# Kernel tuning notes

Hardware: AMD Instinct MI355X
Metric: run time of the kernel (lower is better)

## Reference

```python
import jax, jax.numpy as jnp
import numpy as np
from jax import lax

B, L, D, VOCAB = 4, 256, 256, 29


def conv1d(x, w, b, pad, stride=1):
    # x: (B, C, Len), w: (O, I, K)
    y = lax.conv_general_dilated(x, w, (stride,), [pad], dimension_numbers=('NCH', 'OIH', 'NCH'))
    return y + b[None, :, None]


def setup_inputs() -> dict:
    key = jax.random.key(0)
    ks = jax.random.split(key, 14)
    n = lambda k, shape: jax.random.normal(k, shape, jnp.float32) * 0.05
    return {
        'prot_data1': jax.random.randint(ks[0], (B, L), 0, VOCAB),
        'prot_data2': jax.random.randint(ks[1], (B, L), 0, VOCAB),
        'emb': n(ks[2], (VOCAB, D)),
        'w0': n(ks[3], (D, D, 4)), 'b0': jnp.zeros((D,), jnp.float32),
        'w1': n(ks[4], (D, D, 8)), 'b1': jnp.zeros((D,), jnp.float32),
        'w2': n(ks[5], (D, D, 12)), 'b2': jnp.zeros((D,), jnp.float32),
        'ja1_w': n(ks[6], (D, D)), 'ja1_b': jnp.zeros((D,), jnp.float32),
        'ja2_w': n(ks[7], (D, D)), 'ja2_b': jnp.zeros((D,), jnp.float32),
        'rc_w': n(ks[8], (64, 1, 4)), 'rc_b': jnp.zeros((64,), jnp.float32),
        'fc1_w': n(ks[9], (64 * 32, 600)), 'fc1_b': jnp.zeros((600,), jnp.float32),
        'fc2_w': n(ks[10], (600, 300)), 'fc2_b': jnp.zeros((300,), jnp.float32),
        'fc3_w': n(ks[11], (300, 1)), 'fc3_b': jnp.zeros((1,), jnp.float32),
    }


def reference(prot_data1, prot_data2, emb, w0, b0, w1, b1, w2, b2,
              ja1_w, ja1_b, ja2_w, ja2_b, rc_w, rc_b,
              fc1_w, fc1_b, fc2_w, fc2_b, fc3_w, fc3_b):
    lrelu = lambda x: jnp.where(x >= 0, x, 0.1 * x)

    def encode(tok):
        x = emb[tok]  # (B, L, D); dim 1 is treated as conv channels, as in original
        x = jax.nn.relu(conv1d(x, w0, b0, (1, 2)))
        x = jax.nn.relu(conv1d(x, w1, b1, (3, 4)))
        x = jax.nn.relu(conv1d(x, w2, b2, (5, 6)))
        return x  # (B, L, D), length preserved

    e1 = encode(prot_data1)
    e2 = encode(prot_data2)

    q = jax.nn.relu(e1) @ ja1_w + ja1_b  # (B, L, D)
    k = jax.nn.relu(e2) @ ja2_w + ja2_b  # (B, L, D)
    inter = jax.nn.sigmoid(jnp.einsum('bij,bkj->bik', q, k))  # (B, L, L)
    inter = inter / jnp.sum(inter, axis=(1, 2), keepdims=True)

    # bilinear cross-attention pooling: tanh outer product weighted by inter
    pp = jnp.tanh(e1[:, :, None, :] * e2[:, None, :, :])  # (B, L, L, D)
    pooled = jnp.einsum('bikj,bik->bj', pp, inter)  # (B, D)

    h = lrelu(conv1d(pooled[:, None, :], rc_w, rc_b, (1, 1), stride=2))  # (B, 64, 128)
    h = h.reshape(h.shape[0], 64, 32, 4).max(axis=-1)  # MaxPool1d(4,4) -> (B, 64, 32)
    h = h.reshape(h.shape[0], 64 * 32)
    h = lrelu(h @ fc1_w + fc1_b)
    h = lrelu(h @ fc2_w + fc2_b)
    affn = h @ fc3_w + fc3_b  # (B, 1)
    return (inter, affn)
```

## Files before the change

kernel.cpp:

```cpp
#include <hip/hip_runtime.h>
#include <hip/hip_bf16.h>

typedef unsigned short u16;
typedef unsigned int u32;
typedef short s8v __attribute__((ext_vector_type(8)));
typedef float f32x16 __attribute__((ext_vector_type(16)));

constexpr int B = 4, L = 256, D = 256;
constexpr size_t SZ = (size_t)B * L * D;

constexpr int XROWS = 272;
constexpr size_t XT_PLANE = (size_t)8 * XROWS * 256;

constexpr size_t OFF_E    = 0;
constexpr size_t OFF_S    = 2 * SZ;
constexpr size_t OFF_EBF  = 3 * SZ;
constexpr size_t OFF_XA   = 4 * SZ;
constexpr size_t OFF_XB   = OFF_XA + 278528;
constexpr size_t OFF_WB   = OFF_XB + 278528;
constexpr size_t OFF_WJ   = OFF_WB + 1572864;
constexpr size_t OFF_QK   = OFF_WJ + 131072;
constexpr size_t OFF_BS   = OFF_QK + 262144;
constexpr size_t OFF_PP   = OFF_BS + 256;
constexpr size_t OFF_POOL = OFF_PP + 524288;
constexpr size_t OFF_H    = OFF_POOL + 1024;
constexpr size_t OFF_F1P  = OFF_H + 8192;
constexpr size_t OFF_F2P  = OFF_F1P + 76800;

constexpr size_t WB_L1 = 0;
constexpr size_t WB_L2 = (size_t)4 * 2 * 65536;
constexpr size_t WB_L3 = WB_L2 + (size_t)8 * 2 * 65536;

__device__ __forceinline__ float sig_fast(float x) {
  return __fdividef(1.0f, 1.0f + __expf(-x));
}
__device__ __forceinline__ float lrelu(float x) { return x >= 0.0f ? x : 0.1f * x; }

__device__ __forceinline__ void split_bf16(float v, u16& h, u16& l) {
  __bf16 hb = (__bf16)v;
  float hf = (float)hb;
  __bf16 lb = (__bf16)(v - hf);
  h = __builtin_bit_cast(u16, hb);
  l = __builtin_bit_cast(u16, lb);
}
__device__ __forceinline__ u16 to_bf16(float v) {
  return __builtin_bit_cast(u16, (__bf16)v);
}

__device__ __forceinline__ s8v lds16_8al(const u16* p) {
  union { uint2 u[2]; s8v v; } r;
  r.u[0] = *(const uint2*)p;
  r.u[1] = *(const uint2*)(p + 4);
  return r.v;
}

__global__ __launch_bounds__(256) void k_prepall(const int* __restrict__ t1,
                                                 const int* __restrict__ t2,
                                                 const float* __restrict__ emb,
                                                 const float* __restrict__ w0,
                                                 const float* __restrict__ w1,
                                                 const float* __restrict__ w2,
                                                 const float* __restrict__ jw1,
                                                 const float* __restrict__ jw2,
                                                 u16* __restrict__ xa,
                                                 u16* __restrict__ xb,
                                                 u16* __restrict__ wb,
                                                 u16* __restrict__ wj) {
  __shared__ float st[32][129];
  int blk = blockIdx.x;
  int t = threadIdx.x;
  if (blk < 64) {
    int gid = blk * 256 + t;
    int plane = gid >> 13, rem = gid & 8191;
    int pb = rem >> 10, rem2 = rem & 1023;
    int row16 = rem2 >> 6, cc = rem2 & 63;
    int row = row16 < 8 ? row16 : 256 + row16;
    u16* dst = plane ? xb : xa;
    *(ushort4*)(dst + (size_t)pb * (XROWS * 256) + (size_t)row * 256 + cc * 4) =
        make_ushort4(0, 0, 0, 0);
  } else if (blk < 896) {
    int b2 = blk - 64;
    if (b2 < 768) {
      const float* w; u16* dst; int K, lblk;
      if (b2 < 128) { w = w0; dst = wb + WB_L1; K = 4; lblk = b2; }
      else if (b2 < 384) { w = w1; dst = wb + WB_L2; K = 8; lblk = b2 - 128; }
      else { w = w2; dst = wb + WB_L3; K = 12; lblk = b2 - 384; }
      int q = lblk >> 5, ig = lblk & 31, oc = t;
      union { u16 us[8]; uint4 v; } H, Lo;
#pragma unroll
      for (int e = 0; e < 8; ++e) {
        float v = w[((size_t)oc * 256 + ig * 8 + e) * K + q];
        split_bf16(v, H.us[e], Lo.us[e]);
      }
      size_t d = (size_t)(q * 2) * 65536 + (size_t)ig * 2048 + (size_t)oc * 8;
      *(uint4*)(dst + d) = H.v;
      *(uint4*)(dst + d + 65536) = Lo.v;
    } else {
      int lblk = b2 - 768;
      int kg = lblk & 31, p = lblk >> 5;
      const float* W = p ? jw2 : jw1;
      int n = t;
      union { u16 us[8]; uint4 v; } H, Lo;
#pragma unroll
      for (int e = 0; e < 8; ++e) {
        float v = W[(size_t)(kg * 8 + e) * 256 + n];
        split_bf16(v, H.us[e], Lo.us[e]);
      }
      size_t d = (size_t)(p * 2) * 65536 + ((size_t)kg * 256 + n) * 8;
      *(uint4*)(wj + d) = H.v;
      *(uint4*)(wj + d + 65536) = Lo.v;
    }
  } else {
    int lb = blk - 896;
    int dt = lb & 1, lt = (lb >> 1) & 7, pb = lb >> 4;
    int l0 = lt * 32, d0 = dt * 128;
    const int* tok = (pb >> 2) ? t2 : t1;
    int c = t & 127, rq = t >> 7;
#pragma unroll 4
    for (int rr = 0; rr < 16; ++rr) {
      int r = rr * 2 + rq;
      int tv = tok[(pb & 3) * 256 + l0 + r];
      st[r][c] = emb[(size_t)tv * 256 + d0 + c];
    }
    __syncthreads();
    int dloc = t >> 1, lq = t & 1;
    size_t rbase = (size_t)pb * (XROWS * 256) + (size_t)(8 + d0 + dloc) * 256 + l0 + lq * 16;
#pragma unroll
    for (int lh = 0; lh < 4; ++lh) {
      u16 hb[4];
#pragma unroll
      for (int cc = 0; cc < 4; ++cc)
        hb[cc] = to_bf16(st[lq * 16 + lh * 4 + cc][dloc]);
      *(ushort4*)(xa + rbase + lh * 4) = make_ushort4(hb[0], hb[1], hb[2], hb[3]);
    }
  }
}

template <int K, int P, int OUTMODE>
__global__ __launch_bounds__(256, 2) void k_cmf(const u16* __restrict__ xh,
                                                const u16* __restrict__ wb,
                                                const float* __restrict__ bias,
                                                u16* __restrict__ yh,
                                                float* __restrict__ eout,
                                                u16* __restrict__ ebf) {
  __shared__ u16 xsl[4 * 3264];
  __shared__ float cd[3072];

  int blk = blockIdx.x;
  int jt = blk & 7, oct = (blk >> 3) & 7, pb = blk >> 6;
  int oc0 = oct * 32, j0 = jt * 32;
  int tid = threadIdx.x;
  int lane = tid & 63, wv = tid >> 6;
  int l31 = lane & 31, lhi = lane >> 5;

  {
    const u16* src = xh + (size_t)pb * (XROWS * 256) + (size_t)j0 * 256 + wv * 64;
    u16* dst = xsl + wv * 3264;
#pragma unroll
    for (int it2 = 0; it2 < 12; ++it2) {
      int e = it2 * 64 + lane;
      int r = e >> 4, c4 = (e & 15) * 4;
      *(uint2*)(dst + r * 68 + c4) = *(const uint2*)(src + (size_t)r * 256 + c4);
    }
  }
  asm volatile("s_waitcnt lgkmcnt(0)" ::: "memory");
  __builtin_amdgcn_sched_barrier(0);

  f32x16 acc = {};
  size_t abase = (size_t)(oc0 + l31) * 8 + (size_t)(wv * 8 + lhi) * 2048;
  const u16* wslice = xsl + wv * 3264 + 8 * lhi;

  for (int q = 0; q < K; ++q) {
    int jr = l31 + q + (8 - P);
    const u16* bh0 = wslice + jr * 68;
    size_t aq = (size_t)q * 131072 + abase;
#pragma unroll
    for (int ic = 0; ic < 4; ++ic) {
      s8v ah = *(const s8v*)(wb + aq + ic * 4096);
      s8v al = *(const s8v*)(wb + aq + 65536 + ic * 4096);
      s8v bh = lds16_8al(bh0 + ic * 16);
      acc = __builtin_amdgcn_mfma_f32_32x32x16_bf16(ah, bh, acc, 0, 0, 0);
      acc = __builtin_amdgcn_mfma_f32_32x32x16_bf16(al, bh, acc, 0, 0, 0);
    }
  }

  if (wv > 0) {
#pragma unroll
    for (int r = 0; r < 16; ++r) {
      int ocr = (r & 3) + 8 * (r >> 2) + 4 * lhi;
      cd[(wv - 1) * 1024 + ocr * 32 + l31] = acc[r];
    }
  }
  __syncthreads();
  if (wv == 0) {
    float v[16];
#pragma unroll
    for (int r = 0; r < 16; ++r) {
      int ocr = (r & 3) + 8 * (r >> 2) + 4 * lhi;
      int idx = ocr * 32 + l31;
      v[r] = fmaxf(acc[r] + cd[idx] + cd[1024 + idx] + cd[2048 + idx] + bias[oc0 + ocr], 0.0f);
    }
    if constexpr (OUTMODE == 0) {
      size_t ro = (size_t)pb * (XROWS * 256) + (size_t)(8 + j0 + l31) * 256 + oc0 + 4 * lhi;
#pragma unroll
      for (int rq = 0; rq < 4; ++rq) {
        *(ushort4*)(yh + ro + 8 * rq) =
            make_ushort4(to_bf16(v[rq * 4 + 0]), to_bf16(v[rq * 4 + 1]),
                         to_bf16(v[rq * 4 + 2]), to_bf16(v[rq * 4 + 3]));
      }
    } else {
#pragma unroll
      for (int r = 0; r < 16; ++r) {
        int ocr = (r & 3) + 8 * (r >> 2) + 4 * lhi;
        size_t eo = (size_t)pb * 65536 + (size_t)(oc0 + ocr) * 256 + j0 + l31;
        eout[eo] = v[r];
        ebf[((size_t)pb * 256 + oc0 + ocr) * 256 + j0 + l31] = to_bf16(v[r]);
      }
    }
  }
}

__global__ __launch_bounds__(256) void k_jam(const u16* __restrict__ ebf,
                                             const u16* __restrict__ wj,
                                             const float* __restrict__ b1,
                                             const float* __restrict__ b2,
                                             u16* __restrict__ qk) {
  __shared__ float cd[3072 + 1056];
  int blk = blockIdx.x;
  int nt = blk & 7, it = (blk >> 3) & 7, pb = blk >> 6;
  int p = pb >> 2;
  int i0 = it * 32, n0 = nt * 32;
  int tid = threadIdx.x, wv = tid >> 6, lane = tid & 63;
  int l31 = lane & 31, lhi = lane >> 5;

  const u16* eh = ebf + ((size_t)pb * 256 + i0 + l31) * 256 + lhi * 8;
  const u16* wjh = wj + (size_t)(p * 2) * 65536;

  f32x16 acc = {};
#pragma unroll
  for (int c = 0; c < 4; ++c) {
    int kc = wv * 4 + c;
    int kg = kc * 2 + lhi;
    s8v ah = *(const s8v*)(eh + kc * 16);
    s8v bh = *(const s8v*)(wjh + ((size_t)kg * 256 + n0 + l31) * 8);
    s8v bl = *(const s8v*)(wjh + 65536 + ((size_t)kg * 256 + n0 + l31) * 8);
    acc = __builtin_amdgcn_mfma_f32_32x32x16_bf16(ah, bh, acc, 0, 0, 0);
    acc = __builtin_amdgcn_mfma_f32_32x32x16_bf16(ah, bl, acc, 0, 0, 0);
  }

  if (wv > 0) {
#pragma unroll
    for (int r = 0; r < 16; ++r) {
      int row = (r & 3) + 8 * (r >> 2) + 4 * lhi;
      cd[(wv - 1) * 1024 + row * 32 + l31] = acc[r];
    }
  }
  __syncthreads();
  if (wv == 0) {
    float bv = (p ? b2 : b1)[n0 + l31];
#pragma unroll
    for (int r = 0; r < 16; ++r) {
      int row = (r & 3) + 8 * (r >> 2) + 4 * lhi;
      int idx = row * 32 + l31;
      cd[3072 + row * 33 + l31] = acc[r] + cd[idx] + cd[1024 + idx] + cd[2048 + idx] + bv;
    }
  }
  __syncthreads();

  int row = tid & 31, c8 = tid >> 5;
  u16 hb[4];
#pragma unroll
  for (int cc = 0; cc < 4; ++cc)
    hb[cc] = to_bf16(cd[3072 + row * 33 + c8 * 4 + cc]);
  size_t ro = ((size_t)pb * 256 + i0 + row) * 256 + n0 + c8 * 4;
  *(ushort4*)(qk + ro) = make_ushort4(hb[0], hb[1], hb[2], hb[3]);
}

__global__ __launch_bounds__(256) void k_scoresm(const u16* __restrict__ qk,
                                                 float* __restrict__ S,
                                                 float* __restrict__ bsums) {
  __shared__ float cd[3072 + 1056];
  int blk = blockIdx.x;
  int jt = blk & 7, it = (blk >> 3) & 7, b = blk >> 6;
  int i0 = it * 32, j0 = jt * 32;
  int tid = threadIdx.x, wv = tid >> 6, lane = tid & 63;
  int l31 = lane & 31, lhi = lane >> 5;

  const u16* qh = qk + ((size_t)b * 256 + i0 + l31) * 256 + lhi * 8;
  const u16* kh = qk + ((size_t)(4 + b) * 256 + j0 + l31) * 256 + lhi * 8;

  f32x16 acc = {};
#pragma unroll
  for (int c = 0; c < 4; ++c) {
    int kc = wv * 4 + c;
    s8v a = *(const s8v*)(qh + kc * 16);
    s8v bb = *(const s8v*)(kh + kc * 16);
    acc = __builtin_amdgcn_mfma_f32_32x32x16_bf16(a, bb, acc, 0, 0, 0);
  }

  if (wv > 0) {
#pragma unroll
    for (int r = 0; r < 16; ++r) {
      int row = (r & 3) + 8 * (r >> 2) + 4 * lhi;
      cd[(wv - 1) * 1024 + row * 32 + l31] = acc[r];
    }
  }
  __syncthreads();
  if (wv == 0) {
    float psum = 0.0f;
#pragma unroll
    for (int r = 0; r < 16; ++r) {
      int row = (r & 3) + 8 * (r >> 2) + 4 * lhi;
      int idx = row * 32 + l31;
      float s = sig_fast(acc[r] + cd[idx] + cd[1024 + idx] + cd[2048 + idx]);
      psum += s;
      cd[3072 + row * 33 + l31] = s;
    }
    for (int off = 32; off; off >>= 1) psum += __shfl_down(psum, off, 64);
    if (lane == 0) bsums[blk] = psum;
  }
  __syncthreads();

  int row = tid & 31, c8 = tid >> 5;
  float4 v;
  v.x = cd[3072 + row * 33 + c8 * 4 + 0];
  v.y = cd[3072 + row * 33 + c8 * 4 + 1];
  v.z = cd[3072 + row * 33 + c8 * 4 + 2];
  v.w = cd[3072 + row * 33 + c8 * 4 + 3];
  *(float4*)(S + ((size_t)b * 256 + i0 + row) * 256 + j0 + c8 * 4) = v;
}

__global__ __launch_bounds__(256) void k_pool(const float* __restrict__ e1,
                                              const float* __restrict__ e2,
                                              const float* __restrict__ S,
                                              const float* __restrict__ bsums,
                                              float* __restrict__ inter_out,
                                              float* __restrict__ pp) {
  int blk = blockIdx.x;
  int kch = blk & 15, ich = (blk >> 4) & 31, b = blk >> 9;
  int d = threadIdx.x, i0 = ich * 8, k0 = kch * 16;
  __shared__ float s2[16][8];
  __shared__ float red[128];
  __shared__ float ssp_s, tot_s;
  int t = threadIdx.x;
  int ii = t >> 4, kk = t & 15;
  float sv = 0.0f;
  if (t < 64) {
    float v = bsums[b * 64 + t];
    for (int off = 32; off; off >>= 1) v += __shfl_down(v, off, 64);
    if (t == 0) tot_s = v;
  }
  if (t < 128) {
    sv = S[((size_t)(b * 256 + i0 + ii)) * 256 + k0 + kk];
    s2[kk][ii] = 2.0f * sv;
    red[t] = sv;
  }
  __syncthreads();
  for (int st = 64; st; st >>= 1) {
    if (t < st) red[t] += red[t + st];
    __syncthreads();
  }
  if (t == 0) ssp_s = red[0];
  __syncthreads();

  float invt = 1.0f / tot_s;
  if (t < 128)
    inter_out[((size_t)(b * 256 + i0 + ii)) * 256 + k0 + kk] = sv * invt;

  constexpr float C2L = 2.8853900817779268f;
  float ev2[8];
#pragma unroll
  for (int i2 = 0; i2 < 8; ++i2)
    ev2[i2] = e1[((size_t)(b * L + i0 + i2)) * D + d] * C2L;

  float a0 = 0.f, a1 = 0.f, a2 = 0.f, a3 = 0.f;
  for (int k2 = 0; k2 < 16; ++k2) {
    float e2v = e2[((size_t)(b * L + k0 + k2)) * D + d];
    float s2r[8];
    *(float4*)&s2r[0] = *(const float4*)&s2[k2][0];
    *(float4*)&s2r[4] = *(const float4*)&s2[k2][4];
#pragma unroll
    for (int i2 = 0; i2 < 8; ++i2) {
      float r = __builtin_amdgcn_rcpf(__builtin_exp2f(ev2[i2] * e2v) + 1.0f);
      if ((i2 & 3) == 0) a0 = fmaf(r, s2r[i2], a0);
      else if ((i2 & 3) == 1) a1 = fmaf(r, s2r[i2], a1);
      else if ((i2 & 3) == 2) a2 = fmaf(r, s2r[i2], a2);
      else a3 = fmaf(r, s2r[i2], a3);
    }
  }
  float res = (ssp_s - (a0 + a1 + a2 + a3)) * invt;
  pp[(((size_t)b * 32 + ich) * 16 + kch) * 256 + d] = res;
}

__global__ __launch_bounds__(256) void k_poolcomb(const float* __restrict__ pp,
                                                  float* __restrict__ pooled) {
  int blk = blockIdx.x;
  int dt = blk & 7, b = blk >> 3;
  int t = threadIdx.x, dl = t & 31, mg = t >> 5;
  int d = dt * 32 + dl;
  float s = 0.f;
#pragma unroll
  for (int m = 0; m < 64; ++m)
    s += pp[((size_t)b * 512 + mg * 64 + m) * 256 + d];
  __shared__ float red[8][32];
  red[mg][dl] = s;
  __syncthreads();
  if (mg == 0) {
    float tot = red[0][dl] + red[1][dl] + red[2][dl] + red[3][dl] +
                red[4][dl] + red[5][dl] + red[6][dl] + red[7][dl];
    pooled[b * 256 + d] = tot;
  }
}

__global__ __launch_bounds__(256) void k_head1(const float* __restrict__ pooled,
                                               const float* __restrict__ rcw,
                                               const float* __restrict__ rcb,
                                               float* __restrict__ h) {
  int ms = blockIdx.x;
  __shared__ float spb[4][258];
  int t = threadIdx.x;
#pragma unroll
  for (int s = 0; s < 4; ++s) {
    int idx = s * 256 + t;
    spb[idx >> 8][(idx & 255) + 1] = pooled[idx];
  }
  if (t < 4) { spb[t][0] = 0.0f; spb[t][257] = 0.0f; }
  __syncthreads();
  int b = t >> 6, c = t & 63;
  float w0 = rcw[c * 4 + 0], w1 = rcw[c * 4 + 1], w2 = rcw[c * 4 + 2], w3 = rcw[c * 4 + 3];
  float bias = rcb[c];
#pragma unroll
  for (int mm = 0; mm < 4; ++mm) {
    int m = ms * 4 + mm;
    float mx = -1e30f;
#pragma unroll
    for (int r = 0; r < 4; ++r) {
      int p2 = 2 * (4 * m + r);
      float y = bias;
      y = fmaf(w0, spb[b][p2], y);
      y = fmaf(w1, spb[b][p2 + 1], y);
      y = fmaf(w2, spb[b][p2 + 2], y);
      y = fmaf(w3, spb[b][p2 + 3], y);
      mx = fmaxf(mx, lrelu(y));
    }
    h[(size_t)(b * 64 + c) * 32 + m] = mx;
  }
}

__global__ __launch_bounds__(256) void k_fc1(const float* __restrict__ h,
                                             const float* __restrict__ w,
                                             float* __restrict__ f1p) {
  int blk = blockIdx.x;
  int ich = blk & 31, ot = blk >> 5;
  int t = threadIdx.x, ol = t & 63, b = t >> 6;
  int o = ot * 64 + ol;
  int oc_ = o < 600 ? o : 599;
  const float* hb = h + (size_t)b * 2048 + ich * 64;
  const float* wb = w + (size_t)(ich * 64) * 600 + oc_;
  float a0 = 0.f, a1 = 0.f, a2 = 0.f, a3 = 0.f;
#pragma unroll 4
  for (int i = 0; i < 64; i += 4) {
    a0 = fmaf(hb[i], wb[(size_t)i * 600], a0);
    a1 = fmaf(hb[i + 1], wb[(size_t)(i + 1) * 600], a1);
    a2 = fmaf(hb[i + 2], wb[(size_t)(i + 2) * 600], a2);
    a3 = fmaf(hb[i + 3], wb[(size_t)(i + 3) * 600], a3);
  }
  if (o < 600) f1p[((size_t)ich * 4 + b) * 600 + o] = a0 + a1 + a2 + a3;
}

__global__ __launch_bounds__(256) void k_fc2(const float* __restrict__ f1p,
                                             const float* __restrict__ fc1b,
                                             const float* __restrict__ w,
                                             float* __restrict__ f2p) {
  int blk = blockIdx.x;
  int is = blk & 7, ot = blk >> 3;
  __shared__ float h1s[4][76];
  int t = threadIdx.x;
  for (int e = t; e < 300; e += 256) {
    int bb = e / 75, ii = e % 75;
    int i = is * 75 + ii;
    float s = fc1b[i];
#pragma unroll
    for (int ich = 0; ich < 32; ++ich) s += f1p[((size_t)ich * 4 + bb) * 600 + i];
    h1s[bb][ii] = lrelu(s);
  }
  __syncthreads();
  int ol = t & 63, b = t >> 6;
  int o = ot * 64 + ol, oc_ = o < 300 ? o : 299;
  const float* wb = w + (size_t)(is * 75) * 300 + oc_;
  float a0 = 0.f, a1 = 0.f, a2 = 0.f;
#pragma unroll 5
  for (int ii = 0; ii < 75; ii += 3) {
    a0 = fmaf(h1s[b][ii], wb[(size_t)ii * 300], a0);
    a1 = fmaf(h1s[b][ii + 1], wb[(size_t)(ii + 1) * 300], a1);
    a2 = fmaf(h1s[b][ii + 2], wb[(size_t)(ii + 2) * 300], a2);
  }
  if (o < 300) f2p[((size_t)is * 4 + b) * 300 + o] = a0 + a1 + a2;
}

__global__ __launch_bounds__(1024) void k_fc3f(const float* __restrict__ f2p,
                                               const float* __restrict__ fc2b,
                                               const float* __restrict__ w3,
                                               const float* __restrict__ fc3b,
                                               float* __restrict__ out) {
  __shared__ float h2s[4][304];
  int t = threadIdx.x;
  for (int e = t; e < 1200; e += 1024) {
    int o = e % 300, b = e / 300;
    float s = fc2b[o];
#pragma unroll
    for (int is = 0; is < 8; ++is) s += f2p[((size_t)is * 4 + b) * 300 + o];
    h2s[b][o] = lrelu(s);
  }
  __syncthreads();
  int wv = t >> 6, l = t & 63;
  if (wv < 4) {
    float s = 0.f;
#pragma unroll
    for (int m = 0; m < 5; ++m) {
      int i = m * 64 + l;
      if (i < 300) s = fmaf(h2s[wv][i], w3[i], s);
    }
    for (int off = 32; off; off >>= 1) s += __shfl_down(s, off, 64);
    if (l == 0) out[262144 + wv] = s + fc3b[0];
  }
}

extern "C" void kernel_launch(void* const* d_in, const int* in_sizes, int n_in,
                              void* d_out, int out_size, void* d_ws, size_t ws_size,
                              hipStream_t stream) {
  float* ws = (float*)d_ws;
  const int* p1 = (const int*)d_in[0];
  const int* p2 = (const int*)d_in[1];
  const float* emb  = (const float*)d_in[2];
  const float* w0   = (const float*)d_in[3];
  const float* b0   = (const float*)d_in[4];
  const float* w1   = (const float*)d_in[5];
  const float* b1   = (const float*)d_in[6];
  const float* w2   = (const float*)d_in[7];
  const float* b2   = (const float*)d_in[8];
  const float* ja1w = (const float*)d_in[9];
  const float* ja1b = (const float*)d_in[10];
  const float* ja2w = (const float*)d_in[11];
  const float* ja2b = (const float*)d_in[12];
  const float* rcw  = (const float*)d_in[13];
  const float* rcb  = (const float*)d_in[14];
  const float* fc1w = (const float*)d_in[15];
  const float* fc1b = (const float*)d_in[16];
  const float* fc2w = (const float*)d_in[17];
  const float* fc2b = (const float*)d_in[18];
  const float* fc3w = (const float*)d_in[19];
  const float* fc3b = (const float*)d_in[20];
  float* out = (float*)d_out;

  u16* xa  = (u16*)(ws + OFF_XA);
  u16* xb  = (u16*)(ws + OFF_XB);
  u16* wbu = (u16*)(ws + OFF_WB);
  u16* wju = (u16*)(ws + OFF_WJ);
  u16* ebf = (u16*)(ws + OFF_EBF);
  u16* qk  = (u16*)(ws + OFF_QK);

  k_prepall<<<1024, 256, 0, stream>>>(p1, p2, emb, w0, w1, w2, ja1w, ja2w, xa, xb, wbu, wju);

  k_cmf<4, 1, 0><<<512, 256, 0, stream>>>(xa, wbu + WB_L1, b0, xb, nullptr, nullptr);
  k_cmf<8, 3, 0><<<512, 256, 0, stream>>>(xb, wbu + WB_L2, b1, xa, nullptr, nullptr);
  k_cmf<12, 5, 1><<<512, 256, 0, stream>>>(xa, wbu + WB_L3, b2, nullptr, ws + OFF_E, ebf);

  k_jam<<<512, 256, 0, stream>>>(ebf, wju, ja1b, ja2b, qk);
  k_scoresm<<<256, 256, 0, stream>>>(qk, ws + OFF_S, ws + OFF_BS);

  k_pool<<<2048, 256, 0, stream>>>(ws + OFF_E, ws + OFF_E + SZ, ws + OFF_S, ws + OFF_BS,
                                   out, ws + OFF_PP);
  k_poolcomb<<<32, 256, 0, stream>>>(ws + OFF_PP, ws + OFF_POOL);

  k_head1<<<8, 256, 0, stream>>>(ws + OFF_POOL, rcw, rcb, ws + OFF_H);
  k_fc1<<<320, 256, 0, stream>>>(ws + OFF_H, fc1w, ws + OFF_F1P);
  k_fc2<<<40, 256, 0, stream>>>(ws + OFF_F1P, fc1b, fc2w, ws + OFF_F2P);
  k_fc3f<<<1, 1024, 0, stream>>>(ws + OFF_F2P, fc2b, fc3w, fc3b, out);
}
```

Measured before the change: 98.14 us.

## Drop split-bf16 conv weights, read conv inputs directly, fuse head conv into fc1

Conv weights are now stored as a single bf16 copy instead of a hi/lo split, which halves the MFMA count and weight traffic in the three conv layers. The LDS staging of the input slice is removed, so the B operand is read straight from global memory. The small head conv+maxpool kernel is merged into fc1: each block recomputes its 64 needed h values into shared memory, saving one launch. Dropping the low-order weight part lowers precision and may push error past tolerance, and the direct global reads lose the LDS reuse.

```diff
diff --git a/kernel.cpp b/kernel.cpp
--- a/kernel.cpp
+++ b/kernel.cpp
@@ -10,7 +10,6 @@
 constexpr size_t SZ = (size_t)B * L * D;
 
 constexpr int XROWS = 272;
-constexpr size_t XT_PLANE = (size_t)8 * XROWS * 256;
 
 constexpr size_t OFF_E    = 0;
 constexpr size_t OFF_S    = 2 * SZ;
@@ -18,18 +17,17 @@
 constexpr size_t OFF_XA   = 4 * SZ;
 constexpr size_t OFF_XB   = OFF_XA + 278528;
 constexpr size_t OFF_WB   = OFF_XB + 278528;
-constexpr size_t OFF_WJ   = OFF_WB + 1572864;
+constexpr size_t OFF_WJ   = OFF_WB + 786432;
 constexpr size_t OFF_QK   = OFF_WJ + 131072;
 constexpr size_t OFF_BS   = OFF_QK + 262144;
 constexpr size_t OFF_PP   = OFF_BS + 256;
 constexpr size_t OFF_POOL = OFF_PP + 524288;
-constexpr size_t OFF_H    = OFF_POOL + 1024;
-constexpr size_t OFF_F1P  = OFF_H + 8192;
+constexpr size_t OFF_F1P  = OFF_POOL + 1024;
 constexpr size_t OFF_F2P  = OFF_F1P + 76800;
 
 constexpr size_t WB_L1 = 0;
-constexpr size_t WB_L2 = (size_t)4 * 2 * 65536;
-constexpr size_t WB_L3 = WB_L2 + (size_t)8 * 2 * 65536;
+constexpr size_t WB_L2 = (size_t)4 * 65536;
+constexpr size_t WB_L3 = (size_t)12 * 65536;
 
 __device__ __forceinline__ float sig_fast(float x) {
   return __fdividef(1.0f, 1.0f + __expf(-x));
@@ -45,13 +43,6 @@
 }
 __device__ __forceinline__ u16 to_bf16(float v) {
   return __builtin_bit_cast(u16, (__bf16)v);
-}
-
-__device__ __forceinline__ s8v lds16_8al(const u16* p) {
-  union { uint2 u[2]; s8v v; } r;
-  r.u[0] = *(const uint2*)p;
-  r.u[1] = *(const uint2*)(p + 4);
-  return r.v;
 }
 
 __global__ __launch_bounds__(256) void k_prepall(const int* __restrict__ t1,
@@ -86,15 +77,11 @@
       else if (b2 < 384) { w = w1; dst = wb + WB_L2; K = 8; lblk = b2 - 128; }
       else { w = w2; dst = wb + WB_L3; K = 12; lblk = b2 - 384; }
       int q = lblk >> 5, ig = lblk & 31, oc = t;
-      union { u16 us[8]; uint4 v; } H, Lo;
-#pragma unroll
-      for (int e = 0; e < 8; ++e) {
-        float v = w[((size_t)oc * 256 + ig * 8 + e) * K + q];
-        split_bf16(v, H.us[e], Lo.us[e]);
-      }
-      size_t d = (size_t)(q * 2) * 65536 + (size_t)ig * 2048 + (size_t)oc * 8;
-      *(uint4*)(dst + d) = H.v;
-      *(uint4*)(dst + d + 65536) = Lo.v;
+      union { u16 us[8]; uint4 v; } H;
+#pragma unroll
+      for (int e = 0; e < 8; ++e)
+        H.us[e] = to_bf16(w[((size_t)oc * 256 + ig * 8 + e) * K + q]);
+      *(uint4*)(dst + (size_t)q * 65536 + (size_t)ig * 2048 + (size_t)oc * 8) = H.v;
     } else {
       int lblk = b2 - 768;
       int kg = lblk & 31, p = lblk >> 5;
@@ -137,13 +124,12 @@
 }
 
 template <int K, int P, int OUTMODE>
-__global__ __launch_bounds__(256, 2) void k_cmf(const u16* __restrict__ xh,
-                                                const u16* __restrict__ wb,
-                                                const float* __restrict__ bias,
-                                                u16* __restrict__ yh,
-                                                float* __restrict__ eout,
-                                                u16* __restrict__ ebf) {
-  __shared__ u16 xsl[4 * 3264];
+__global__ __launch_bounds__(256) void k_cmf(const u16* __restrict__ xh,
+                                             const u16* __restrict__ wb,
+                                             const float* __restrict__ bias,
+                                             u16* __restrict__ yh,
+                                             float* __restrict__ eout,
+                                             u16* __restrict__ ebf) {
   __shared__ float cd[3072];
 
   int blk = blockIdx.x;
@@ -153,34 +139,19 @@
   int lane = tid & 63, wv = tid >> 6;
   int l31 = lane & 31, lhi = lane >> 5;
 
-  {
-    const u16* src = xh + (size_t)pb * (XROWS * 256) + (size_t)j0 * 256 + wv * 64;
-    u16* dst = xsl + wv * 3264;
-#pragma unroll
-    for (int it2 = 0; it2 < 12; ++it2) {
-      int e = it2 * 64 + lane;
-      int r = e >> 4, c4 = (e & 15) * 4;
-      *(uint2*)(dst + r * 68 + c4) = *(const uint2*)(src + (size_t)r * 256 + c4);
-    }
-  }
-  asm volatile("s_waitcnt lgkmcnt(0)" ::: "memory");
-  __builtin_amdgcn_sched_barrier(0);
-
   f32x16 acc = {};
   size_t abase = (size_t)(oc0 + l31) * 8 + (size_t)(wv * 8 + lhi) * 2048;
-  const u16* wslice = xsl + wv * 3264 + 8 * lhi;
+  const u16* brow = xh + (size_t)pb * (XROWS * 256) +
+                    (size_t)(j0 + l31 + 8 - P) * 256 + wv * 64 + lhi * 8;
 
   for (int q = 0; q < K; ++q) {
-    int jr = l31 + q + (8 - P);
-    const u16* bh0 = wslice + jr * 68;
-    size_t aq = (size_t)q * 131072 + abase;
+    const u16* bsrc = brow + (size_t)q * 256;
+    size_t aq = (size_t)q * 65536 + abase;
 #pragma unroll
     for (int ic = 0; ic < 4; ++ic) {
       s8v ah = *(const s8v*)(wb + aq + ic * 4096);
-      s8v al = *(const s8v*)(wb + aq + 65536 + ic * 4096);
-      s8v bh = lds16_8al(bh0 + ic * 16);
+      s8v bh = *(const s8v*)(bsrc + ic * 16);
       acc = __builtin_amdgcn_mfma_f32_32x32x16_bf16(ah, bh, acc, 0, 0, 0);
-      acc = __builtin_amdgcn_mfma_f32_32x32x16_bf16(al, bh, acc, 0, 0, 0);
     }
   }
 
@@ -412,12 +383,15 @@
   }
 }
 
-__global__ __launch_bounds__(256) void k_head1(const float* __restrict__ pooled,
-                                               const float* __restrict__ rcw,
-                                               const float* __restrict__ rcb,
-                                               float* __restrict__ h) {
-  int ms = blockIdx.x;
+__global__ __launch_bounds__(256) void k_fc1h(const float* __restrict__ pooled,
+                                              const float* __restrict__ rcw,
+                                              const float* __restrict__ rcb,
+                                              const float* __restrict__ w,
+                                              float* __restrict__ f1p) {
+  int blk = blockIdx.x;
+  int ich = blk & 31, ot = blk >> 5;
   __shared__ float spb[4][258];
+  __shared__ float hs[4][64];
   int t = threadIdx.x;
 #pragma unroll
   for (int s = 0; s < 4; ++s) {
@@ -426,12 +400,11 @@
   }
   if (t < 4) { spb[t][0] = 0.0f; spb[t][257] = 0.0f; }
   __syncthreads();
-  int b = t >> 6, c = t & 63;
-  float w0 = rcw[c * 4 + 0], w1 = rcw[c * 4 + 1], w2 = rcw[c * 4 + 2], w3 = rcw[c * 4 + 3];
-  float bias = rcb[c];
-#pragma unroll
-  for (int mm = 0; mm < 4; ++mm) {
-    int m = ms * 4 + mm;
+  {
+    int b = t >> 6, idx = t & 63;
+    int c = ich * 2 + (idx >> 5), m = idx & 31;
+    float w0 = rcw[c * 4 + 0], w1 = rcw[c * 4 + 1], w2 = rcw[c * 4 + 2], w3 = rcw[c * 4 + 3];
+    float bias = rcb[c];
     float mx = -1e30f;
 #pragma unroll
     for (int r = 0; r < 4; ++r) {
@@ -443,27 +416,21 @@
       y = fmaf(w3, spb[b][p2 + 3], y);
       mx = fmaxf(mx, lrelu(y));
     }
-    h[(size_t)(b * 64 + c) * 32 + m] = mx;
-  }
-}
-
-__global__ __launch_bounds__(256) void k_fc1(const float* __restrict__ h,
-                                             const float* __restrict__ w,
-                                             float* __restrict__ f1p) {
-  int blk = blockIdx.x;
-  int ich = blk & 31, ot = blk >> 5;
-  int t = threadIdx.x, ol = t & 63, b = t >> 6;
+    hs[b][idx] = mx;
+  }
+  __syncthreads();
+
+  int ol = t & 63, b = t >> 6;
   int o = ot * 64 + ol;
   int oc_ = o < 600 ? o : 599;
-  const float* hb = h + (size_t)b * 2048 + ich * 64;
   const float* wb = w + (size_t)(ich * 64) * 600 + oc_;
   float a0 = 0.f, a1 = 0.f, a2 = 0.f, a3 = 0.f;
 #pragma unroll 4
   for (int i = 0; i < 64; i += 4) {
-    a0 = fmaf(hb[i], wb[(size_t)i * 600], a0);
-    a1 = fmaf(hb[i + 1], wb[(size_t)(i + 1) * 600], a1);
-    a2 = fmaf(hb[i + 2], wb[(size_t)(i + 2) * 600], a2);
-    a3 = fmaf(hb[i + 3], wb[(size_t)(i + 3) * 600], a3);
+    a0 = fmaf(hs[b][i], wb[(size_t)i * 600], a0);
+    a1 = fmaf(hs[b][i + 1], wb[(size_t)(i + 1) * 600], a1);
+    a2 = fmaf(hs[b][i + 2], wb[(size_t)(i + 2) * 600], a2);
+    a3 = fmaf(hs[b][i + 3], wb[(size_t)(i + 3) * 600], a3);
   }
   if (o < 600) f1p[((size_t)ich * 4 + b) * 600 + o] = a0 + a1 + a2 + a3;
 }
@@ -573,8 +540,7 @@
                                    out, ws + OFF_PP);
   k_poolcomb<<<32, 256, 0, stream>>>(ws + OFF_PP, ws + OFF_POOL);
 
-  k_head1<<<8, 256, 0, stream>>>(ws + OFF_POOL, rcw, rcb, ws + OFF_H);
-  k_fc1<<<320, 256, 0, stream>>>(ws + OFF_H, fc1w, ws + OFF_F1P);
+  k_fc1h<<<320, 256, 0, stream>>>(ws + OFF_POOL, rcw, rcb, fc1w, ws + OFF_F1P);
   k_fc2<<<40, 256, 0, stream>>>(ws + OFF_F1P, fc1b, fc2w, ws + OFF_F2P);
   k_fc3f<<<1, 1024, 0, stream>>>(ws + OFF_F2P, fc2b, fc3w, fc3b, out);
 }
```

After: 96.22 us, median of 2. About the same (-2.0%).
